# Kernel optimization log

Hardware: AMD Instinct MI355X
Metric: run time of the kernel (lower is better)

## Reference

```python
import jax, jax.numpy as jnp
import numpy as np

# Module config (matches init_kwargs)
H, W, C = 32, 32, 256
K = 3                      # filter_size
B = 16
TEMP = 1.0                 # softmax_temp
CH, CW = H - K + 1, W - K + 1   # convs_height/width (valid padding, stride 1)
NF = CH * CW               # num_convs
FS = K * K                 # filter_size squared (window size)
HW = H * W


def _local_indices():
    # flattened (row-major over H,W) positions of each KxK window, sorted ascending
    idx = np.zeros((NF, FS), dtype=np.int32)
    c = 0
    for i in range(CH):
        for j in range(CW):
            win = [(i + di) * W + (j + dj) for di in range(K) for dj in range(K)]
            idx[c] = np.sort(win)
            c += 1
    return jnp.asarray(idx)


def setup_inputs() -> dict:
    key = jax.random.key(0)
    ks = jax.random.split(key, 7)
    s = 1.0 / np.sqrt(C)  # torch Linear default init scale
    return {
        "batch": jax.random.normal(ks[0], (B, C, H, W), dtype=jnp.float32),
        "key_w": jax.random.uniform(ks[1], (C, C), jnp.float32, -s, s),
        "key_b": jax.random.uniform(ks[2], (C,), jnp.float32, -s, s),
        "query_w": jax.random.uniform(ks[3], (C, C), jnp.float32, -s, s),
        "query_b": jax.random.uniform(ks[4], (C,), jnp.float32, -s, s),
        "value_w": jax.random.uniform(ks[5], (1, C), jnp.float32, -s, s),
        "value_b": jax.random.uniform(ks[6], (1,), jnp.float32, -s, s),
        "local_indices": _local_indices(),
    }


def _normalize(t):
    # F.normalize(dim=-1), eps=1e-12
    return t / jnp.maximum(jnp.linalg.norm(t, axis=-1, keepdims=True), 1e-12)


def reference(batch, key_w, key_b, query_w, query_b, value_w, value_b, local_indices):
    # [B,C,H,W] -> [B,HW,C]
    x = batch.transpose(0, 2, 3, 1).reshape(B, HW, C)
    # local patches: X_l[f,b,k,c] = x[b, local_indices[f,k], c]  -> [NF,B,FS,C]
    X_l = x[:, local_indices].transpose(1, 0, 2, 3)
    # global is the full (unmasked) feature map: X_g = x  -> [B,HW,C]
    keys = x @ key_w.T + key_b                       # [B,HW,C]
    queries = X_l @ query_w.T + query_b              # [NF,B,FS,C]
    values = (x @ value_w.T + value_b)[..., 0]       # [B,HW]
    # cosine similarity: [NF,B,HW,FS]
    comp = jnp.einsum('bnc,fbkc->fbnk', _normalize(keys), _normalize(queries))
    att = jax.nn.softmax(TEMP * comp, axis=2)        # softmax over HW
    # W_g[f,b,k] = sum_n values[b,n] * att[f,b,n,k]
    W_g = jnp.einsum('bn,fbnk->fbk', values, att)
    # convolved: sum over window positions, weighted
    conv = jnp.einsum('fbk,fbkc->fbc', W_g, X_l)     # [NF,B,C]
    out = conv.transpose(1, 0, 2).reshape(B, CH, CW, C).transpose(0, 3, 1, 2)
    return out  # [B,C,CH,CW]
```

## Files before the change

kernel.cpp:

```cpp
#include <hip/hip_runtime.h>
#include <hip/hip_bf16.h>


#define NB 16
#define NC 256
#define NHW 1024
#define NCH 30

typedef __attribute__((ext_vector_type(8))) short short8;
typedef __attribute__((ext_vector_type(4))) float f32x4;

static __device__ __forceinline__ unsigned short f2bf(float f) {
    __hip_bfloat16 h = __float2bfloat16(f);
    return *(unsigned short*)&h;
}
static __device__ __forceinline__ float bf2f(unsigned short u) {
    unsigned int x = ((unsigned int)u) << 16;
    return __uint_as_float(x);
}

__global__ __launch_bounds__(256) void wconv_kernel(
    const float* __restrict__ key_w, const float* __restrict__ query_w,
    unsigned short* __restrict__ kwb, unsigned short* __restrict__ qwb)
{
    const int gx = blockIdx.x, t = threadIdx.x;
    const float* src = (gx < 16) ? key_w : query_w;
    unsigned short* dst = (gx < 16) ? kwb : qwb;
    int base = (gx & 15) * 4096;
    #pragma unroll
    for (int k = 0; k < 4; ++k) {
        int i = base + (k * 256 + t) * 4;
        float4 a = *(const float4*)(src + i);
        ushort4 o;
        o.x = f2bf(a.x); o.y = f2bf(a.y); o.z = f2bf(a.z); o.w = f2bf(a.w);
        *(ushort4*)(dst + i) = o;
    }
}

__global__ __launch_bounds__(512, 2) void fused_lin_kernel(
    const float* __restrict__ batch,
    const float* __restrict__ value_w, const float* __restrict__ value_b,
    const unsigned short* __restrict__ kwb, const unsigned short* __restrict__ qwb,
    const float* __restrict__ key_b, const float* __restrict__ query_b,
    unsigned short* __restrict__ xc,
    unsigned short* __restrict__ Kn, unsigned short* __restrict__ Qn,
    float* __restrict__ vout)
{
    const int b = blockIdx.y, n0 = blockIdx.x * 64;
    const int t = threadIdx.x, wave = t >> 6, lane = t & 63;
    const int nw = wave & 3, ch = wave >> 2;
    const int l15 = lane & 15, quad = lane >> 4;

    __shared__ float Xs[2][64][65];
    __shared__ float PK[2][4][16], PQ[2][4][16];
    __shared__ float4 vred[8][16];

    const int c_l = t >> 4;
    const int n4  = (t & 15) * 4;
    const float* bb = batch + (size_t)b * NC * NHW + n0;
    unsigned short* xcp = xc + (size_t)b * NC * NHW + n0;
    float4 vacc = {0.f, 0.f, 0.f, 0.f};

    const short* kbase = (const short*)kwb + (size_t)(ch * 128 + l15) * NC + quad * 8;
    const short* qbase = (const short*)qwb + (size_t)(ch * 128 + l15) * NC + quad * 8;

    short8 wK[2][8], wQ[2][8];
    #pragma unroll
    for (int ct = 0; ct < 8; ++ct) {
        wK[0][ct] = *(const short8*)(kbase + ct * 16 * NC);
        wQ[0][ct] = *(const short8*)(qbase + ct * 16 * NC);
    }

    float4 x0, x1;
    {
        int c0 = c_l, c1 = c_l + 32;
        x0 = *(const float4*)(bb + (size_t)c0 * NHW + n4);
        x1 = *(const float4*)(bb + (size_t)c1 * NHW + n4);
        ushort4 o0, o1;
        o0.x = f2bf(x0.x); o0.y = f2bf(x0.y); o0.z = f2bf(x0.z); o0.w = f2bf(x0.w);
        o1.x = f2bf(x1.x); o1.y = f2bf(x1.y); o1.z = f2bf(x1.z); o1.w = f2bf(x1.w);
        *(ushort4*)(xcp + (size_t)c0 * NHW + n4) = o0;
        *(ushort4*)(xcp + (size_t)c1 * NHW + n4) = o1;
        float w0 = value_w[c0], w1 = value_w[c1];
        vacc.x += x0.x * w0 + x1.x * w1; vacc.y += x0.y * w0 + x1.y * w1;
        vacc.z += x0.z * w0 + x1.z * w1; vacc.w += x0.w * w0 + x1.w * w1;
        float* r0 = &Xs[0][c_l][n4];
        r0[0] = x0.x; r0[1] = x0.y; r0[2] = x0.z; r0[3] = x0.w;
        float* r1 = &Xs[0][c_l + 32][n4];
        r1[0] = x1.x; r1[1] = x1.y; r1[2] = x1.z; r1[3] = x1.w;
    }
    __syncthreads();

    f32x4 accK[8], accQ[8];
    #pragma unroll
    for (int ct = 0; ct < 8; ++ct) {
        int co = ch * 128 + ct * 16 + l15;
        float bK = key_b[co], bQ = query_b[co];
        accK[ct] = (f32x4){bK, bK, bK, bK};
        accQ[ct] = (f32x4){bQ, bQ, bQ, bQ};
    }

    for (int cc = 0; cc < 4; ++cc) {
        if (cc < 3) {
            int c0 = (cc + 1) * 64 + c_l, c1 = c0 + 32;
            x0 = *(const float4*)(bb + (size_t)c0 * NHW + n4);
            x1 = *(const float4*)(bb + (size_t)c1 * NHW + n4);
            ushort4 o0, o1;
            o0.x = f2bf(x0.x); o0.y = f2bf(x0.y); o0.z = f2bf(x0.z); o0.w = f2bf(x0.w);
            o1.x = f2bf(x1.x); o1.y = f2bf(x1.y); o1.z = f2bf(x1.z); o1.w = f2bf(x1.w);
            *(ushort4*)(xcp + (size_t)c0 * NHW + n4) = o0;
            *(ushort4*)(xcp + (size_t)c1 * NHW + n4) = o1;
            float w0 = value_w[c0], w1 = value_w[c1];
            vacc.x += x0.x * w0 + x1.x * w1; vacc.y += x0.y * w0 + x1.y * w1;
            vacc.z += x0.z * w0 + x1.z * w1; vacc.w += x0.w * w0 + x1.w * w1;
        }
        const int cur = cc & 1;
        #pragma unroll
        for (int kc = 0; kc < 2; ++kc) {
            const int g = cc * 2 + kc;
            if (g < 7) {
                const int nb_ = (g + 1) & 1;
                #pragma unroll
                for (int ct = 0; ct < 8; ++ct) {
                    wK[nb_][ct] = *(const short8*)(kbase + ct * 16 * NC + (g + 1) * 32);
                    wQ[nb_][ct] = *(const short8*)(qbase + ct * 16 * NC + (g + 1) * 32);
                }
            }
            short8 af;
            #pragma unroll
            for (int j = 0; j < 8; ++j)
                af[j] = (short)f2bf(Xs[cur][kc * 32 + quad * 8 + j][nw * 16 + l15]);
            const int cb = g & 1;
            #pragma unroll
            for (int ct = 0; ct < 8; ++ct) {
                accK[ct] = __builtin_amdgcn_mfma_f32_16x16x32_bf16(af, wK[cb][ct], accK[ct], 0, 0, 0);
                accQ[ct] = __builtin_amdgcn_mfma_f32_16x16x32_bf16(af, wQ[cb][ct], accQ[ct], 0, 0, 0);
            }
        }
        if (cc < 3) {
            const int nxt = (cc + 1) & 1;
            float* r0 = &Xs[nxt][c_l][n4];
            r0[0] = x0.x; r0[1] = x0.y; r0[2] = x0.z; r0[3] = x0.w;
            float* r1 = &Xs[nxt][c_l + 32][n4];
            r1[0] = x1.x; r1[1] = x1.y; r1[2] = x1.z; r1[3] = x1.w;
            __syncthreads();
        }
    }

    vacc.x += __shfl_xor(vacc.x, 16, 64); vacc.x += __shfl_xor(vacc.x, 32, 64);
    vacc.y += __shfl_xor(vacc.y, 16, 64); vacc.y += __shfl_xor(vacc.y, 32, 64);
    vacc.z += __shfl_xor(vacc.z, 16, 64); vacc.z += __shfl_xor(vacc.z, 32, 64);
    vacc.w += __shfl_xor(vacc.w, 16, 64); vacc.w += __shfl_xor(vacc.w, 32, 64);

    float nK[4] = {0, 0, 0, 0}, nQ[4] = {0, 0, 0, 0};
    #pragma unroll
    for (int ct = 0; ct < 8; ++ct)
        #pragma unroll
        for (int r = 0; r < 4; ++r) {
            nK[r] += accK[ct][r] * accK[ct][r];
            nQ[r] += accQ[ct][r] * accQ[ct][r];
        }
    #pragma unroll
    for (int r = 0; r < 4; ++r)
        #pragma unroll
        for (int o = 1; o < 16; o <<= 1) {
            nK[r] += __shfl_xor(nK[r], o, 64);
            nQ[r] += __shfl_xor(nQ[r], o, 64);
        }
    if (l15 == 0)
        #pragma unroll
        for (int r = 0; r < 4; ++r) {
            PK[ch][nw][quad * 4 + r] = nK[r];
            PQ[ch][nw][quad * 4 + r] = nQ[r];
        }
    if (lane < 16) vred[wave][l15] = vacc;
    __syncthreads();

    float ik[4], iq[4];
    #pragma unroll
    for (int r = 0; r < 4; ++r) {
        float sk = PK[0][nw][quad * 4 + r] + PK[1][nw][quad * 4 + r];
        float sq = PQ[0][nw][quad * 4 + r] + PQ[1][nw][quad * 4 + r];
        ik[r] = 1.f / fmaxf(sqrtf(sk), 1e-12f);
        iq[r] = 1.f / fmaxf(sqrtf(sq), 1e-12f);
    }
    #pragma unroll
    for (int ct = 0; ct < 8; ++ct)
        #pragma unroll
        for (int r = 0; r < 4; ++r) {
            size_t row = (size_t)(b * NHW + n0 + nw * 16 + quad * 4 + r) * NC
                       + ch * 128 + ct * 16 + l15;
            Kn[row] = f2bf(accK[ct][r] * ik[r]);
            Qn[row] = f2bf(accQ[ct][r] * iq[r]);
        }
    if (t < 16) {
        float4 s = {0.f, 0.f, 0.f, 0.f};
        #pragma unroll
        for (int w = 0; w < 8; ++w) {
            float4 p = vred[w][t];
            s.x += p.x; s.y += p.y; s.z += p.z; s.w += p.w;
        }
        float vb = value_b[0];
        s.x += vb; s.y += vb; s.z += vb; s.w += vb;
        *(float4*)(vout + b * NHW + n0 + t * 4) = s;
    }
}

__global__ __launch_bounds__(512) void attn_kernel(
    const unsigned short* __restrict__ Kn,
    const unsigned short* __restrict__ Qn,
    const float* __restrict__ vbuf,
    float* __restrict__ R)
{
    const int b = blockIdx.y, m0 = blockIdx.x * 64;
    const int t = threadIdx.x, wave = t >> 6, lane = t & 63;
    const int l15 = lane & 15, quad = lane >> 4;

    short8 bf[4][8];
    #pragma unroll
    for (int ms = 0; ms < 4; ++ms) {
        const short* q = (const short*)Qn
                       + (size_t)(b * NHW + m0 + ms * 16 + l15) * NC + quad * 8;
        #pragma unroll
        for (int c = 0; c < 8; ++c) bf[ms][c] = *(const short8*)(q + 32 * c);
    }
    const float* vb = vbuf + b * NHW;
    const int nstart = wave * 128;
    const short* ka = (const short*)Kn + (size_t)(b * NHW + nstart + l15) * NC + quad * 8;

    float z[4] = {0.f, 0.f, 0.f, 0.f}, tc[4] = {0.f, 0.f, 0.f, 0.f};
    for (int it = 0; it < 8; ++it, ka += 16 * NC) {
        short8 af[8];
        #pragma unroll
        for (int c = 0; c < 8; ++c) af[c] = *(const short8*)(ka + 32 * c);
        f32x4 a0[4], a1[4];
        #pragma unroll
        for (int ms = 0; ms < 4; ++ms) { a0[ms] = (f32x4){0,0,0,0}; a1[ms] = (f32x4){0,0,0,0}; }
        #pragma unroll
        for (int c = 0; c < 4; ++c)
            #pragma unroll
            for (int ms = 0; ms < 4; ++ms) {
                a0[ms] = __builtin_amdgcn_mfma_f32_16x16x32_bf16(af[c],     bf[ms][c],     a0[ms], 0, 0, 0);
                a1[ms] = __builtin_amdgcn_mfma_f32_16x16x32_bf16(af[c + 4], bf[ms][c + 4], a1[ms], 0, 0, 0);
            }
        float4 vv = *(const float4*)(vb + nstart + it * 16 + quad * 4);
        #pragma unroll
        for (int ms = 0; ms < 4; ++ms)
            #pragma unroll
            for (int r = 0; r < 4; ++r) {
                float e = __expf(a0[ms][r] + a1[ms][r]);
                z[ms] += e;
                tc[ms] += ((const float*)&vv)[r] * e;
            }
    }
    #pragma unroll
    for (int ms = 0; ms < 4; ++ms) {
        z[ms]  += __shfl_xor(z[ms], 16, 64);  z[ms]  += __shfl_xor(z[ms], 32, 64);
        tc[ms] += __shfl_xor(tc[ms], 16, 64); tc[ms] += __shfl_xor(tc[ms], 32, 64);
    }

    __shared__ float zs[8][4][16], ts[8][4][16];
    if (lane < 16)
        #pragma unroll
        for (int ms = 0; ms < 4; ++ms) {
            zs[wave][ms][l15] = z[ms];
            ts[wave][ms][l15] = tc[ms];
        }
    __syncthreads();
    if (t < 64) {
        int ms = t >> 4, li = t & 15;
        float zz = 0.f, tt = 0.f;
        #pragma unroll
        for (int w = 0; w < 8; ++w) { zz += zs[w][ms][li]; tt += ts[w][ms][li]; }
        R[b * NHW + m0 + ms * 16 + li] = tt / zz;
    }
}

__global__ __launch_bounds__(256) void out_kernel(
    const unsigned short* __restrict__ xc,
    const float* __restrict__ R,
    float* __restrict__ out)
{
    const int bc = blockIdx.x;
    const int b  = bc >> 8;
    const int t  = threadIdx.x;
    __shared__ float P[NHW];

    const unsigned short* xp = xc + (size_t)bc * NHW;
    const float* rp = R + b * NHW;
    {
        ushort4 xv = *(const ushort4*)(xp + t * 4);
        float4  rv = *(const float4*)(rp + t * 4);
        P[t * 4 + 0] = rv.x * bf2f(xv.x);
        P[t * 4 + 1] = rv.y * bf2f(xv.y);
        P[t * 4 + 2] = rv.z * bf2f(xv.z);
        P[t * 4 + 3] = rv.w * bf2f(xv.w);
    }
    __syncthreads();
    for (int idx = t; idx < NCH * NCH; idx += 256) {
        int i = idx / NCH, j = idx - i * NCH;
        const float* pr = &P[i * 32 + j];
        float s = pr[0]  + pr[1]  + pr[2]
                + pr[32] + pr[33] + pr[34]
                + pr[64] + pr[65] + pr[66];
        out[(size_t)bc * (NCH * NCH) + idx] = s;
    }
}

extern "C" void kernel_launch(void* const* d_in, const int* in_sizes, int n_in,
                              void* d_out, int out_size, void* d_ws, size_t ws_size,
                              hipStream_t stream) {
    const float* batch   = (const float*)d_in[0];
    const float* key_w   = (const float*)d_in[1];
    const float* key_b   = (const float*)d_in[2];
    const float* query_w = (const float*)d_in[3];
    const float* query_b = (const float*)d_in[4];
    const float* value_w = (const float*)d_in[5];
    const float* value_b = (const float*)d_in[6];
    float* out = (float*)d_out;

    char* ws = (char*)d_ws;
    const size_t KQ = (size_t)NB * NHW * NC;
    unsigned short* xc  = (unsigned short*)ws;
    unsigned short* Kn  = xc + KQ;
    unsigned short* Qn  = Kn + KQ;
    unsigned short* kwb = Qn + KQ;
    unsigned short* qwb = kwb + NC * NC;
    float* vbuf = (float*)(qwb + NC * NC);
    float* Rbuf = vbuf + NB * NHW;

    wconv_kernel<<<32, 256, 0, stream>>>(key_w, query_w, kwb, qwb);
    fused_lin_kernel<<<dim3(16, NB), 512, 0, stream>>>(batch, value_w, value_b,
                                                       kwb, qwb, key_b, query_b,
                                                       xc, Kn, Qn, vbuf);
    attn_kernel<<<dim3(16, NB), 512, 0, stream>>>(Kn, Qn, vbuf, Rbuf);
    out_kernel<<<NB * NC, 256, 0, stream>>>(xc, Rbuf, out);
}
```

Before: 147.6 us.

## Retile linear projection kernel to 16-position blocks with pre-packed MFMA weights

The fused key/query projection kernel now processes 16 spatial positions per 256-thread block (1024 blocks instead of 256), with each wave owning 64 output channels. Weights are pre-packed into MFMA fragment order so each lane loads contiguous short8 values, and the input tile is staged in LDS as transposed bf16, so the A fragment is a single vector LDS read instead of eight scalar reads with conversions. The goal is more blocks for better CU occupancy and cheaper fragment loads. In exchange, every block re-reads the full weight matrices, which adds more L2 weight traffic.

```diff
diff --git a/kernel.cpp b/kernel.cpp
--- a/kernel.cpp
+++ b/kernel.cpp
@@ -21,98 +21,94 @@
 
 __global__ __launch_bounds__(256) void wconv_kernel(
     const float* __restrict__ key_w, const float* __restrict__ query_w,
-    unsigned short* __restrict__ kwb, unsigned short* __restrict__ qwb)
+    unsigned short* __restrict__ kpk, unsigned short* __restrict__ qpk)
 {
-    const int gx = blockIdx.x, t = threadIdx.x;
-    const float* src = (gx < 16) ? key_w : query_w;
-    unsigned short* dst = (gx < 16) ? kwb : qwb;
-    int base = (gx & 15) * 4096;
-    #pragma unroll
-    for (int k = 0; k < 4; ++k) {
-        int i = base + (k * 256 + t) * 4;
-        float4 a = *(const float4*)(src + i);
-        ushort4 o;
-        o.x = f2bf(a.x); o.y = f2bf(a.y); o.z = f2bf(a.z); o.w = f2bf(a.w);
-        *(ushort4*)(dst + i) = o;
-    }
-}
-
-__global__ __launch_bounds__(512, 2) void fused_lin_kernel(
+    const int gx = blockIdx.x;
+    const int mat = gx >> 3, g = gx & 7, t = threadIdx.x;
+    const float* src = mat ? query_w : key_w;
+    unsigned short* dst = mat ? qpk : kpk;
+    #pragma unroll
+    for (int it = 0; it < 4; ++it) {
+        int idx = it * 256 + t;
+        int ct = idx >> 6, lane = idx & 63;
+        int l15 = lane & 15, q = lane >> 4;
+        const float* s = src + (ct * 16 + l15) * NC + g * 32 + q * 8;
+        float4 a = *(const float4*)s;
+        float4 c = *(const float4*)(s + 4);
+        short8 o;
+        o[0] = (short)f2bf(a.x); o[1] = (short)f2bf(a.y);
+        o[2] = (short)f2bf(a.z); o[3] = (short)f2bf(a.w);
+        o[4] = (short)f2bf(c.x); o[5] = (short)f2bf(c.y);
+        o[6] = (short)f2bf(c.z); o[7] = (short)f2bf(c.w);
+        *(short8*)(dst + ((size_t)(g * 16 + ct) * 64 + lane) * 8) = o;
+    }
+}
+
+__global__ __launch_bounds__(256, 4) void fused_lin_kernel(
     const float* __restrict__ batch,
     const float* __restrict__ value_w, const float* __restrict__ value_b,
-    const unsigned short* __restrict__ kwb, const unsigned short* __restrict__ qwb,
+    const unsigned short* __restrict__ kpk, const unsigned short* __restrict__ qpk,
     const float* __restrict__ key_b, const float* __restrict__ query_b,
     unsigned short* __restrict__ xc,
     unsigned short* __restrict__ Kn, unsigned short* __restrict__ Qn,
     float* __restrict__ vout)
 {
-    const int b = blockIdx.y, n0 = blockIdx.x * 64;
+    const int b = blockIdx.y, n0 = blockIdx.x * 16;
     const int t = threadIdx.x, wave = t >> 6, lane = t & 63;
-    const int nw = wave & 3, ch = wave >> 2;
     const int l15 = lane & 15, quad = lane >> 4;
 
-    __shared__ float Xs[2][64][65];
-    __shared__ float PK[2][4][16], PQ[2][4][16];
-    __shared__ float4 vred[8][16];
-
-    const int c_l = t >> 4;
-    const int n4  = (t & 15) * 4;
+    __shared__ unsigned short Xs[2][16][72];
+    __shared__ float PK[4][16], PQ[4][16];
+    __shared__ float4 vred[4][4];
+
+    const int c_l = t >> 2;
+    const int n4  = (t & 3) * 4;
     const float* bb = batch + (size_t)b * NC * NHW + n0;
     unsigned short* xcp = xc + (size_t)b * NC * NHW + n0;
     float4 vacc = {0.f, 0.f, 0.f, 0.f};
 
-    const short* kbase = (const short*)kwb + (size_t)(ch * 128 + l15) * NC + quad * 8;
-    const short* qbase = (const short*)qwb + (size_t)(ch * 128 + l15) * NC + quad * 8;
-
-    short8 wK[2][8], wQ[2][8];
-    #pragma unroll
-    for (int ct = 0; ct < 8; ++ct) {
-        wK[0][ct] = *(const short8*)(kbase + ct * 16 * NC);
-        wQ[0][ct] = *(const short8*)(qbase + ct * 16 * NC);
-    }
-
-    float4 x0, x1;
+    const unsigned short* kbase = kpk + (size_t)(wave * 4) * 512 + lane * 8;
+    const unsigned short* qbase = qpk + (size_t)(wave * 4) * 512 + lane * 8;
+
+    short8 wK[2][4], wQ[2][4];
+    #pragma unroll
+    for (int ct = 0; ct < 4; ++ct) {
+        wK[0][ct] = *(const short8*)(kbase + ct * 512);
+        wQ[0][ct] = *(const short8*)(qbase + ct * 512);
+    }
+
     {
-        int c0 = c_l, c1 = c_l + 32;
-        x0 = *(const float4*)(bb + (size_t)c0 * NHW + n4);
-        x1 = *(const float4*)(bb + (size_t)c1 * NHW + n4);
-        ushort4 o0, o1;
+        float4 x0 = *(const float4*)(bb + (size_t)c_l * NHW + n4);
+        ushort4 o0;
         o0.x = f2bf(x0.x); o0.y = f2bf(x0.y); o0.z = f2bf(x0.z); o0.w = f2bf(x0.w);
-        o1.x = f2bf(x1.x); o1.y = f2bf(x1.y); o1.z = f2bf(x1.z); o1.w = f2bf(x1.w);
-        *(ushort4*)(xcp + (size_t)c0 * NHW + n4) = o0;
-        *(ushort4*)(xcp + (size_t)c1 * NHW + n4) = o1;
-        float w0 = value_w[c0], w1 = value_w[c1];
-        vacc.x += x0.x * w0 + x1.x * w1; vacc.y += x0.y * w0 + x1.y * w1;
-        vacc.z += x0.z * w0 + x1.z * w1; vacc.w += x0.w * w0 + x1.w * w1;
-        float* r0 = &Xs[0][c_l][n4];
-        r0[0] = x0.x; r0[1] = x0.y; r0[2] = x0.z; r0[3] = x0.w;
-        float* r1 = &Xs[0][c_l + 32][n4];
-        r1[0] = x1.x; r1[1] = x1.y; r1[2] = x1.z; r1[3] = x1.w;
+        *(ushort4*)(xcp + (size_t)c_l * NHW + n4) = o0;
+        float w0 = value_w[c_l];
+        vacc.x += x0.x * w0; vacc.y += x0.y * w0;
+        vacc.z += x0.z * w0; vacc.w += x0.w * w0;
+        Xs[0][n4 + 0][c_l] = o0.x; Xs[0][n4 + 1][c_l] = o0.y;
+        Xs[0][n4 + 2][c_l] = o0.z; Xs[0][n4 + 3][c_l] = o0.w;
     }
     __syncthreads();
 
-    f32x4 accK[8], accQ[8];
-    #pragma unroll
-    for (int ct = 0; ct < 8; ++ct) {
-        int co = ch * 128 + ct * 16 + l15;
+    f32x4 accK[4], accQ[4];
+    #pragma unroll
+    for (int ct = 0; ct < 4; ++ct) {
+        int co = wave * 64 + ct * 16 + l15;
         float bK = key_b[co], bQ = query_b[co];
         accK[ct] = (f32x4){bK, bK, bK, bK};
         accQ[ct] = (f32x4){bQ, bQ, bQ, bQ};
     }
 
     for (int cc = 0; cc < 4; ++cc) {
+        ushort4 o0;
         if (cc < 3) {
-            int c0 = (cc + 1) * 64 + c_l, c1 = c0 + 32;
-            x0 = *(const float4*)(bb + (size_t)c0 * NHW + n4);
-            x1 = *(const float4*)(bb + (size_t)c1 * NHW + n4);
-            ushort4 o0, o1;
+            int c0 = (cc + 1) * 64 + c_l;
+            float4 x0 = *(const float4*)(bb + (size_t)c0 * NHW + n4);
             o0.x = f2bf(x0.x); o0.y = f2bf(x0.y); o0.z = f2bf(x0.z); o0.w = f2bf(x0.w);
-            o1.x = f2bf(x1.x); o1.y = f2bf(x1.y); o1.z = f2bf(x1.z); o1.w = f2bf(x1.w);
             *(ushort4*)(xcp + (size_t)c0 * NHW + n4) = o0;
-            *(ushort4*)(xcp + (size_t)c1 * NHW + n4) = o1;
-            float w0 = value_w[c0], w1 = value_w[c1];
-            vacc.x += x0.x * w0 + x1.x * w1; vacc.y += x0.y * w0 + x1.y * w1;
-            vacc.z += x0.z * w0 + x1.z * w1; vacc.w += x0.w * w0 + x1.w * w1;
+            float w0 = value_w[c0];
+            vacc.x += x0.x * w0; vacc.y += x0.y * w0;
+            vacc.z += x0.z * w0; vacc.w += x0.w * w0;
         }
         const int cur = cc & 1;
         #pragma unroll
@@ -121,40 +117,39 @@
             if (g < 7) {
                 const int nb_ = (g + 1) & 1;
                 #pragma unroll
-                for (int ct = 0; ct < 8; ++ct) {
-                    wK[nb_][ct] = *(const short8*)(kbase + ct * 16 * NC + (g + 1) * 32);
-                    wQ[nb_][ct] = *(const short8*)(qbase + ct * 16 * NC + (g + 1) * 32);
+                for (int ct = 0; ct < 4; ++ct) {
+                    wK[nb_][ct] = *(const short8*)(kbase + (g + 1) * 8192 + ct * 512);
+                    wQ[nb_][ct] = *(const short8*)(qbase + (g + 1) * 8192 + ct * 512);
                 }
             }
-            short8 af;
-            #pragma unroll
-            for (int j = 0; j < 8; ++j)
-                af[j] = (short)f2bf(Xs[cur][kc * 32 + quad * 8 + j][nw * 16 + l15]);
+            short8 af = *(const short8*)&Xs[cur][l15][kc * 32 + quad * 8];
             const int cb = g & 1;
             #pragma unroll
-            for (int ct = 0; ct < 8; ++ct) {
+            for (int ct = 0; ct < 4; ++ct) {
                 accK[ct] = __builtin_amdgcn_mfma_f32_16x16x32_bf16(af, wK[cb][ct], accK[ct], 0, 0, 0);
                 accQ[ct] = __builtin_amdgcn_mfma_f32_16x16x32_bf16(af, wQ[cb][ct], accQ[ct], 0, 0, 0);
             }
         }
         if (cc < 3) {
             const int nxt = (cc + 1) & 1;
-            float* r0 = &Xs[nxt][c_l][n4];
-            r0[0] = x0.x; r0[1] = x0.y; r0[2] = x0.z; r0[3] = x0.w;
-            float* r1 = &Xs[nxt][c_l + 32][n4];
-            r1[0] = x1.x; r1[1] = x1.y; r1[2] = x1.z; r1[3] = x1.w;
+            Xs[nxt][n4 + 0][c_l] = o0.x; Xs[nxt][n4 + 1][c_l] = o0.y;
+            Xs[nxt][n4 + 2][c_l] = o0.z; Xs[nxt][n4 + 3][c_l] = o0.w;
             __syncthreads();
         }
     }
 
+    vacc.x += __shfl_xor(vacc.x, 4, 64); vacc.x += __shfl_xor(vacc.x, 8, 64);
     vacc.x += __shfl_xor(vacc.x, 16, 64); vacc.x += __shfl_xor(vacc.x, 32, 64);
+    vacc.y += __shfl_xor(vacc.y, 4, 64); vacc.y += __shfl_xor(vacc.y, 8, 64);
     vacc.y += __shfl_xor(vacc.y, 16, 64); vacc.y += __shfl_xor(vacc.y, 32, 64);
+    vacc.z += __shfl_xor(vacc.z, 4, 64); vacc.z += __shfl_xor(vacc.z, 8, 64);
     vacc.z += __shfl_xor(vacc.z, 16, 64); vacc.z += __shfl_xor(vacc.z, 32, 64);
+    vacc.w += __shfl_xor(vacc.w, 4, 64); vacc.w += __shfl_xor(vacc.w, 8, 64);
     vacc.w += __shfl_xor(vacc.w, 16, 64); vacc.w += __shfl_xor(vacc.w, 32, 64);
 
     float nK[4] = {0, 0, 0, 0}, nQ[4] = {0, 0, 0, 0};
     #pragma unroll
-    for (int ct = 0; ct < 8; ++ct)
+    for (int ct = 0; ct < 4; ++ct)
         #pragma unroll
         for (int r = 0; r < 4; ++r) {
             nK[r] += accK[ct][r] * accK[ct][r];
@@ -170,33 +165,34 @@
     if (l15 == 0)
         #pragma unroll
         for (int r = 0; r < 4; ++r) {
-            PK[ch][nw][quad * 4 + r] = nK[r];
-            PQ[ch][nw][quad * 4 + r] = nQ[r];
-        }
-    if (lane < 16) vred[wave][l15] = vacc;
+            PK[wave][quad * 4 + r] = nK[r];
+            PQ[wave][quad * 4 + r] = nQ[r];
+        }
+    if (lane < 4) vred[wave][lane] = vacc;
     __syncthreads();
 
     float ik[4], iq[4];
     #pragma unroll
     for (int r = 0; r < 4; ++r) {
-        float sk = PK[0][nw][quad * 4 + r] + PK[1][nw][quad * 4 + r];
-        float sq = PQ[0][nw][quad * 4 + r] + PQ[1][nw][quad * 4 + r];
+        int qr = quad * 4 + r;
+        float sk = PK[0][qr] + PK[1][qr] + PK[2][qr] + PK[3][qr];
+        float sq = PQ[0][qr] + PQ[1][qr] + PQ[2][qr] + PQ[3][qr];
         ik[r] = 1.f / fmaxf(sqrtf(sk), 1e-12f);
         iq[r] = 1.f / fmaxf(sqrtf(sq), 1e-12f);
     }
     #pragma unroll
-    for (int ct = 0; ct < 8; ++ct)
+    for (int ct = 0; ct < 4; ++ct)
         #pragma unroll
         for (int r = 0; r < 4; ++r) {
-            size_t row = (size_t)(b * NHW + n0 + nw * 16 + quad * 4 + r) * NC
-                       + ch * 128 + ct * 16 + l15;
+            size_t row = (size_t)(b * NHW + n0 + quad * 4 + r) * NC
+                       + wave * 64 + ct * 16 + l15;
             Kn[row] = f2bf(accK[ct][r] * ik[r]);
             Qn[row] = f2bf(accQ[ct][r] * iq[r]);
         }
-    if (t < 16) {
+    if (t < 4) {
         float4 s = {0.f, 0.f, 0.f, 0.f};
         #pragma unroll
-        for (int w = 0; w < 8; ++w) {
+        for (int w = 0; w < 4; ++w) {
             float4 p = vred[w][t];
             s.x += p.x; s.y += p.y; s.z += p.z; s.w += p.w;
         }
@@ -324,14 +320,14 @@
     unsigned short* xc  = (unsigned short*)ws;
     unsigned short* Kn  = xc + KQ;
     unsigned short* Qn  = Kn + KQ;
-    unsigned short* kwb = Qn + KQ;
-    unsigned short* qwb = kwb + NC * NC;
-    float* vbuf = (float*)(qwb + NC * NC);
+    unsigned short* kpk = Qn + KQ;
+    unsigned short* qpk = kpk + NC * NC;
+    float* vbuf = (float*)(qpk + NC * NC);
     float* Rbuf = vbuf + NB * NHW;
 
-    wconv_kernel<<<32, 256, 0, stream>>>(key_w, query_w, kwb, qwb);
-    fused_lin_kernel<<<dim3(16, NB), 512, 0, stream>>>(batch, value_w, value_b,
-                                                       kwb, qwb, key_b, query_b,
+    wconv_kernel<<<16, 256, 0, stream>>>(key_w, query_w, kpk, qpk);
+    fused_lin_kernel<<<dim3(64, NB), 256, 0, stream>>>(batch, value_w, value_b,
+                                                       kpk, qpk, key_b, query_b,
                                                        xc, Kn, Qn, vbuf);
     attn_kernel<<<dim3(16, NB), 512, 0, stream>>>(Kn, Qn, vbuf, Rbuf);
     out_kernel<<<NB * NC, 256, 0, stream>>>(xc, Rbuf, out);
```

After: 132.3 us. 10.4% less time.
